# Optimization experiments

Measured on AMD Instinct MI355X. Metric: run time of the kernel, lower is better.

## Reference

```python
import jax, jax.numpy as jnp
import numpy as np
from jax import lax

B, H, W = 32, 40, 256
FREQ = 40            # freq_num
WIND = 0.5           # wind_size (seconds)
KF = 5               # input_filter_kernel (odd -> 'same' length)
CNN_OUT = 64 * 36 * 252  # out_channels[-1] * (H-4) * (W-4)


def setup_inputs() -> dict:
    key = jax.random.key(0)
    ks = jax.random.split(key, 9)
    return {
        "inputs": jax.random.normal(ks[0], (B, 1, H, W), jnp.float32),
        "w0": jax.random.normal(ks[1], (32, 1, 3, 3), jnp.float32) * 0.1,
        "b0": jax.random.normal(ks[2], (32,), jnp.float32) * 0.05,
        "w1": jax.random.normal(ks[3], (64, 32, 3, 3), jnp.float32) * 0.05,
        "b1": jax.random.normal(ks[4], (64,), jnp.float32) * 0.05,
        "wf": jax.random.normal(ks[5], (1, 1, 1, KF), jnp.float32) * 0.2,
        "bf": jax.random.normal(ks[6], (1,), jnp.float32) * 0.05,
        "wr": jax.random.normal(ks[7], (FREQ, CNN_OUT), jnp.float32) * 1e-3,
        "br": jax.random.normal(ks[8], (FREQ,), jnp.float32) * 0.05,
    }


def _conv2d(x, w, padding):
    return lax.conv_general_dilated(
        x, w, window_strides=(1, 1), padding=padding,
        dimension_numbers=("NCHW", "OIHW", "NCHW"))


def reference(inputs, w0, b0, w1, b1, wf, bf, wr, br):
    b, _, h, w_len = inputs.shape
    # input_filter: Conv1d(1,1,KF, padding=KF//2) applied independently per
    # frequency row -> equivalent to a 2D conv with a (1,KF) kernel.
    p = KF // 2
    feats = _conv2d(inputs, wf, [(0, 0), (p, p)]) + bf[None, :, None, None]  # [B,1,H,W]

    # conv stack with ReLU
    x = jax.nn.relu(_conv2d(inputs, w0, "VALID") + b0[None, :, None, None])
    x = jax.nn.relu(_conv2d(x, w1, "VALID") + b1[None, :, None, None])

    gates = jax.nn.sigmoid(x.reshape(b, -1) @ wr.T + br)

    fs = (1.0 / WIND) * jnp.linspace(1.0, FREQ, FREQ)          # [FREQ]
    wtd_mean_mod = jnp.mean(gates * fs[None, :])               # scalar

    # Fused modulation transform: instead of the per-frequency python loop
    # with materialized [B,H,W] broadcasts, compute sin/cos bases [FREQ,W]
    # and reduce over time with a single einsum each.
    t = jnp.linspace(0.0, WIND, w_len)                          # [W]
    phase = (2.0 * np.pi) * fs[:, None] * t[None, :]            # [FREQ,W]
    f0 = feats[:, 0]                                            # [B,H,W]
    inv_w = jnp.float32(1.0 / w_len)
    sins = jnp.einsum("fw,bhw->bfh", jnp.sin(phase), f0) * inv_w  # mean over W
    coss = jnp.einsum("fw,bhw->bfh", jnp.cos(phase), f0) * inv_w
    mag = jnp.sqrt(sins * sins + coss * coss)                   # [B,FREQ,H]
    mods = (mag * gates[:, :, None]).reshape(b, FREQ * h)       # cat over freq, dim=1
    return mods, wtd_mean_mod
```

## Files before the change

### kernel.cpp

```cpp
#include <hip/hip_runtime.h>
#include <hip/hip_bf16.h>
#include <math.h>

#define BB   32
#define HH   40
#define WW   256
#define NF   40
#define H1N  36
#define W1N  252
#define KCNN 580608
#define NW2  2016
#define KPW  288

typedef __attribute__((ext_vector_type(8))) short bf16x8;
typedef __attribute__((ext_vector_type(4))) float f32x4;

static __device__ __forceinline__ unsigned short f2bf(float v) {
    __hip_bfloat16 h = __float2bfloat16(v);
    return *(unsigned short*)&h;
}

static __device__ __forceinline__ bf16x8 packbf(float4 lo, float4 hi) {
    bf16x8 r;
    r[0] = (short)f2bf(lo.x); r[1] = (short)f2bf(lo.y);
    r[2] = (short)f2bf(lo.z); r[3] = (short)f2bf(lo.w);
    r[4] = (short)f2bf(hi.x); r[5] = (short)f2bf(hi.y);
    r[6] = (short)f2bf(hi.z); r[7] = (short)f2bf(hi.w);
    return r;
}

__global__ void k0_prep_w1(const float* __restrict__ w1, unsigned short* __restrict__ w1c) {
    int o = blockIdx.x * 256 + threadIdx.x;
    int c0  = o & 31;
    int c1  = (o >> 5) & 63;
    int tap = o >> 11;
    w1c[o] = f2bf(w1[(c1 * 32 + c0) * 9 + tap]);
}

__global__ __launch_bounds__(256) void k1_conv(
        const float* __restrict__ inp, const float* __restrict__ w0,
        const float* __restrict__ b0, const unsigned short* __restrict__ w1c,
        const float* __restrict__ b1, unsigned short* __restrict__ xbf) {
    __shared__ float ins[8 * 68];
    __shared__ __align__(16) unsigned short y0T[396 * 40];

    const int jt = blockIdx.x;
    const int it = blockIdx.y;
    const int b  = blockIdx.z;
    const int i0 = it * 4;
    const int j0 = jt * 64;
    const int tid = threadIdx.x;

    for (int s = tid; s < 544; s += 256) {
        int r = s / 68, c = s - r * 68;
        int gc = j0 + c;
        ins[s] = (gc < WW) ? inp[(b * HH + i0 + r) * WW + gc] : 0.0f;
    }
    __syncthreads();

    {
        const int c0 = tid & 31;
        const int pg = tid >> 5;
        float wreg[9];
        #pragma unroll
        for (int k = 0; k < 9; ++k) wreg[k] = w0[c0 * 9 + k];
        const float bias = b0[c0];
        for (int it2 = 0; it2 < 50; ++it2) {
            int pos = it2 * 8 + pg;
            if (pos < 396) {
                int r   = pos / 66;
                int col = pos - r * 66;
                float v = 0.0f;
                if (j0 + col < 254) {
                    float a = bias;
                    #pragma unroll
                    for (int ki = 0; ki < 3; ++ki)
                        #pragma unroll
                        for (int kj = 0; kj < 3; ++kj)
                            a = fmaf(ins[(r + ki) * 68 + col + kj], wreg[ki * 3 + kj], a);
                    v = fmaxf(a, 0.0f);
                }
                y0T[pos * 40 + c0] = f2bf(v);
            }
        }
    }
    __syncthreads();

    const int w    = tid >> 6;
    const int lane = tid & 63;
    const int l15  = lane & 15;
    const int quad = lane >> 4;

    float biasr[4][4];
    #pragma unroll
    for (int mt = 0; mt < 4; ++mt)
        #pragma unroll
        for (int rg = 0; rg < 4; ++rg)
            biasr[mt][rg] = b1[mt * 16 + quad * 4 + rg];

    f32x4 acc[4][4];
    #pragma unroll
    for (int mt = 0; mt < 4; ++mt)
        #pragma unroll
        for (int nt = 0; nt < 4; ++nt)
            acc[mt][nt] = (f32x4){0.f, 0.f, 0.f, 0.f};

    #pragma unroll
    for (int ki = 0; ki < 3; ++ki) {
        #pragma unroll
        for (int kj = 0; kj < 3; ++kj) {
            const int tap = ki * 3 + kj;
            bf16x8 af[4], bfr[4];
            #pragma unroll
            for (int mt = 0; mt < 4; ++mt)
                af[mt] = *(const bf16x8*)(w1c + ((tap * 64 + mt * 16 + l15) * 32 + quad * 8));
            #pragma unroll
            for (int nt = 0; nt < 4; ++nt)
                bfr[nt] = *(const bf16x8*)(y0T + (((w + ki) * 66 + nt * 16 + l15 + kj) * 40 + quad * 8));
            #pragma unroll
            for (int mt = 0; mt < 4; ++mt)
                #pragma unroll
                for (int nt = 0; nt < 4; ++nt)
                    acc[mt][nt] = __builtin_amdgcn_mfma_f32_16x16x32_bf16(
                        af[mt], bfr[nt], acc[mt][nt], 0, 0, 0);
        }
    }

    const int irow = i0 + w;
    #pragma unroll
    for (int nt = 0; nt < 4; ++nt) {
        const int j = j0 + nt * 16 + l15;
        if (j < W1N) {
            #pragma unroll
            for (int mt = 0; mt < 4; ++mt) {
                #pragma unroll
                for (int rg = 0; rg < 4; ++rg) {
                    int c1 = mt * 16 + quad * 4 + rg;
                    float v = fmaxf(acc[mt][nt][rg] + biasr[mt][rg], 0.0f);
                    xbf[(size_t)b * KCNN + (c1 * H1N + irow) * W1N + j] = f2bf(v);
                }
            }
        }
    }
}

__global__ __launch_bounds__(512) void k2_gemm(
        const unsigned short* __restrict__ xbf, const float* __restrict__ wr,
        float* __restrict__ gacc) {
    __shared__ float red[8][32][41];

    const int tid  = threadIdx.x;
    const int wv   = tid >> 6;
    const int lane = tid & 63;
    const int l15  = lane & 15;
    const int quad = lane >> 4;
    const size_t kw = (size_t)(blockIdx.x * 8 + wv) * KPW;

    const unsigned short* ap0 = xbf + (size_t)l15 * KCNN + kw + quad * 8;
    const unsigned short* ap1 = ap0 + (size_t)16 * KCNN;
    const float* bp0 = wr + (size_t)l15 * KCNN + kw + quad * 8;
    const float* bp1 = bp0 + (size_t)16 * KCNN;
    const bool v2 = (l15 < 8);
    const float* bp2 = bp0 + (size_t)32 * KCNN;

    f32x4 acc[2][3];
    #pragma unroll
    for (int mt = 0; mt < 2; ++mt)
        #pragma unroll
        for (int nt = 0; nt < 3; ++nt)
            acc[mt][nt] = (f32x4){0.f, 0.f, 0.f, 0.f};

    const float4 fz = {0.f, 0.f, 0.f, 0.f};
    bf16x8 a0c, a1c, a0n, a1n;
    float4 bw[3][2], bwn[3][2];

    a0c = *(const bf16x8*)ap0;
    a1c = *(const bf16x8*)ap1;
    bw[0][0] = *(const float4*)bp0; bw[0][1] = *(const float4*)(bp0 + 4);
    bw[1][0] = *(const float4*)bp1; bw[1][1] = *(const float4*)(bp1 + 4);
    if (v2) { bw[2][0] = *(const float4*)bp2; bw[2][1] = *(const float4*)(bp2 + 4); }
    else    { bw[2][0] = fz; bw[2][1] = fz; }

    for (int c = 0; c < 9; ++c) {
        if (c < 8) {
            const int o2 = (c + 1) * 32;
            a0n = *(const bf16x8*)(ap0 + o2);
            a1n = *(const bf16x8*)(ap1 + o2);
            bwn[0][0] = *(const float4*)(bp0 + o2); bwn[0][1] = *(const float4*)(bp0 + o2 + 4);
            bwn[1][0] = *(const float4*)(bp1 + o2); bwn[1][1] = *(const float4*)(bp1 + o2 + 4);
            if (v2) { bwn[2][0] = *(const float4*)(bp2 + o2); bwn[2][1] = *(const float4*)(bp2 + o2 + 4); }
            else    { bwn[2][0] = fz; bwn[2][1] = fz; }
        }
        #pragma unroll
        for (int nt = 0; nt < 3; ++nt) {
            bf16x8 bfrag = packbf(bw[nt][0], bw[nt][1]);
            acc[0][nt] = __builtin_amdgcn_mfma_f32_16x16x32_bf16(a0c, bfrag, acc[0][nt], 0, 0, 0);
            acc[1][nt] = __builtin_amdgcn_mfma_f32_16x16x32_bf16(a1c, bfrag, acc[1][nt], 0, 0, 0);
        }
        if (c < 8) {
            a0c = a0n; a1c = a1n;
            #pragma unroll
            for (int nt = 0; nt < 3; ++nt) { bw[nt][0] = bwn[nt][0]; bw[nt][1] = bwn[nt][1]; }
        }
    }

    #pragma unroll
    for (int mt = 0; mt < 2; ++mt)
        #pragma unroll
        for (int nt = 0; nt < 3; ++nt)
            #pragma unroll
            for (int rg = 0; rg < 4; ++rg) {
                int bb = mt * 16 + quad * 4 + rg;
                int ff = nt * 16 + l15;
                if (ff < NF) red[wv][bb][ff] = acc[mt][nt][rg];
            }
    __syncthreads();
    for (int p = tid; p < 1280; p += 512) {
        int bb = p / 40, ff = p - bb * 40;
        float s = 0.0f;
        #pragma unroll
        for (int w = 0; w < 8; ++w) s += red[w][bb][ff];
        atomicAdd(gacc + p, s);
    }
}

__global__ void k3_gates(const float* __restrict__ gacc, const float* __restrict__ br,
                         float* __restrict__ gates, float* __restrict__ out) {
    int p = blockIdx.x * 64 + threadIdx.x;
    int f = p % 40;
    float g = 1.0f / (1.0f + __expf(-(gacc[p] + br[f])));
    gates[p] = g;
    float fs = 2.0f * (float)(f + 1);
    atomicAdd(out + 51200, g * fs * (1.0f / 1280.0f));
}

__global__ __launch_bounds__(320) void k4_mods(
        const float* __restrict__ inp, const float* __restrict__ wf,
        const float* __restrict__ bfp, const float* __restrict__ gates,
        float* __restrict__ out) {
    const int f = blockIdx.x, b = blockIdx.y;
    const int tid = threadIdx.x;
    const int h  = tid >> 3;
    const int wl = tid & 7;
    float wfv[5];
    #pragma unroll
    for (int t = 0; t < 5; ++t) wfv[t] = wf[t];
    const float bias = bfp[0];
    const float cph = 6.283185307179586f * (float)(f + 1) / 255.0f;
    const float* row = inp + (b * HH + h) * WW;
    float sa = 0.0f, ca = 0.0f;
    for (int m = 0; m < 32; ++m) {
        int w = wl + 8 * m;
        float feat = bias;
        #pragma unroll
        for (int d = -2; d <= 2; ++d) {
            int wc = w + d;
            if (wc >= 0 && wc < WW) feat = fmaf(row[wc], wfv[d + 2], feat);
        }
        float sv, cv;
        __sincosf(cph * (float)w, &sv, &cv);
        sa = fmaf(sv, feat, sa);
        ca = fmaf(cv, feat, ca);
    }
    #pragma unroll
    for (int off = 4; off >= 1; off >>= 1) {
        sa += __shfl_xor(sa, off, 8);
        ca += __shfl_xor(ca, off, 8);
    }
    if (wl == 0) {
        float mag = sqrtf(sa * sa + ca * ca) * (1.0f / 256.0f);
        out[b * 1600 + f * 40 + h] = mag * gates[b * 40 + f];
    }
}

extern "C" void kernel_launch(void* const* d_in, const int* in_sizes, int n_in,
                              void* d_out, int out_size, void* d_ws, size_t ws_size,
                              hipStream_t stream) {
    const float* inp = (const float*)d_in[0];
    const float* w0  = (const float*)d_in[1];
    const float* b0  = (const float*)d_in[2];
    const float* w1  = (const float*)d_in[3];
    const float* b1  = (const float*)d_in[4];
    const float* wf  = (const float*)d_in[5];
    const float* bf_ = (const float*)d_in[6];
    const float* wr  = (const float*)d_in[7];
    const float* br  = (const float*)d_in[8];
    float* out = (float*)d_out;

    char* ws = (char*)d_ws;
    unsigned short* xbf = (unsigned short*)ws;
    unsigned short* w1c = (unsigned short*)(ws + 37158912);
    float* gacc  = (float*)(ws + 37195776);
    float* gates = (float*)(ws + 37200896);

    k0_prep_w1<<<72, 256, 0, stream>>>(w1, w1c);
    hipMemsetAsync(gacc, 0, 1280 * 4, stream);
    hipMemsetAsync(out + 51200, 0, 4, stream);
    k1_conv<<<dim3(4, 9, 32), 256, 0, stream>>>(inp, w0, b0, w1c, b1, xbf);
    k2_gemm<<<252, 512, 0, stream>>>(xbf, wr, gacc);
    k3_gates<<<20, 64, 0, stream>>>(gacc, br, gates, out);
    k4_mods<<<dim3(40, 32), 320, 0, stream>>>(inp, wf, bf_, gates, out);
}
```

Before: 233.0 us.

## Fuse gate epilogue into GEMM, stage conv output through LDS, drop memsets

Several changes land together. The gates/sigmoid kernel and both memsets are removed: k0 zeroes the accumulators, and the last-finishing GEMM block, found through an atomic counter, computes the gates and the weighted mean. The conv1 output is staged in shared memory and written with vectorized coalesced stores instead of scattered 2-byte stores. Conv0 now uses a register sliding window over rows, and the GEMM uses 504 blocks of 256 threads with branch-free loads on the third weight tile. These aim to cut launch overhead and uncoalesced global writes, at the cost of a serialized tail in one block and extra syncs.

```diff
diff --git a/kernel.cpp b/kernel.cpp
--- a/kernel.cpp
+++ b/kernel.cpp
@@ -9,7 +9,7 @@
 #define H1N  36
 #define W1N  252
 #define KCNN 580608
-#define NW2  2016
+#define NBLK2 504
 #define KPW  288
 
 typedef __attribute__((ext_vector_type(8))) short bf16x8;
@@ -29,20 +29,27 @@
     return r;
 }
 
-__global__ void k0_prep_w1(const float* __restrict__ w1, unsigned short* __restrict__ w1c) {
+__global__ void k0_prep(const float* __restrict__ w1, unsigned short* __restrict__ w1c,
+                        float* __restrict__ gacc, unsigned int* __restrict__ done) {
     int o = blockIdx.x * 256 + threadIdx.x;
     int c0  = o & 31;
     int c1  = (o >> 5) & 63;
     int tap = o >> 11;
     w1c[o] = f2bf(w1[(c1 * 32 + c0) * 9 + tap]);
+    if (blockIdx.x == 71) {
+        for (int p = threadIdx.x; p < 1280; p += 256) gacc[p] = 0.0f;
+        if (threadIdx.x == 0) *done = 0u;
+    }
 }
 
 __global__ __launch_bounds__(256) void k1_conv(
         const float* __restrict__ inp, const float* __restrict__ w0,
         const float* __restrict__ b0, const unsigned short* __restrict__ w1c,
         const float* __restrict__ b1, unsigned short* __restrict__ xbf) {
-    __shared__ float ins[8 * 68];
-    __shared__ __align__(16) unsigned short y0T[396 * 40];
+    __shared__ __align__(16) unsigned short smem[18432];
+    unsigned short* y0T = smem;
+    float* ins = (float*)(smem + 15840);
+    unsigned short* xp = smem;
 
     const int jt = blockIdx.x;
     const int it = blockIdx.y;
@@ -51,36 +58,60 @@
     const int j0 = jt * 64;
     const int tid = threadIdx.x;
 
-    for (int s = tid; s < 544; s += 256) {
+    for (int s = tid; s < 546; s += 256) {
         int r = s / 68, c = s - r * 68;
-        int gc = j0 + c;
-        ins[s] = (gc < WW) ? inp[(b * HH + i0 + r) * WW + gc] : 0.0f;
+        float v = 0.0f;
+        if (r < 8 && (j0 + c) < WW) v = inp[(b * HH + i0 + r) * WW + j0 + c];
+        ins[s] = v;
     }
     __syncthreads();
 
     {
-        const int c0 = tid & 31;
-        const int pg = tid >> 5;
+        const int c0  = tid & 31;
+        const int sub = tid >> 5;
         float wreg[9];
         #pragma unroll
         for (int k = 0; k < 9; ++k) wreg[k] = w0[c0 * 9 + k];
         const float bias = b0[c0];
-        for (int it2 = 0; it2 < 50; ++it2) {
-            int pos = it2 * 8 + pg;
-            if (pos < 396) {
-                int r   = pos / 66;
-                int col = pos - r * 66;
-                float v = 0.0f;
-                if (j0 + col < 254) {
-                    float a = bias;
+        for (int s = sub; s < 17; s += 8) {
+            const int cbase = 4 * s;
+            float rows[3][6];
+            #pragma unroll
+            for (int r = 0; r < 8; ++r) {
+                {
+                    const float4 a  = *(const float4*)&ins[r * 68 + cbase];
+                    const float2 b2 = *(const float2*)&ins[r * 68 + cbase + 4];
+                    float* dst = rows[r % 3];
+                    dst[0] = a.x; dst[1] = a.y; dst[2] = a.z;
+                    dst[3] = a.w; dst[4] = b2.x; dst[5] = b2.y;
+                }
+                if (r >= 2) {
+                    const int ro = r - 2;
+                    const float* r0 = rows[ro % 3];
+                    const float* r1 = rows[(ro + 1) % 3];
+                    const float* r2 = rows[(ro + 2) % 3];
                     #pragma unroll
-                    for (int ki = 0; ki < 3; ++ki)
-                        #pragma unroll
-                        for (int kj = 0; kj < 3; ++kj)
-                            a = fmaf(ins[(r + ki) * 68 + col + kj], wreg[ki * 3 + kj], a);
-                    v = fmaxf(a, 0.0f);
+                    for (int c = 0; c < 4; ++c) {
+                        const int colg = cbase + c;
+                        if (colg < 66) {
+                            float v = 0.0f;
+                            if (j0 + colg < 254) {
+                                float a = bias;
+                                a = fmaf(r0[c],     wreg[0], a);
+                                a = fmaf(r0[c + 1], wreg[1], a);
+                                a = fmaf(r0[c + 2], wreg[2], a);
+                                a = fmaf(r1[c],     wreg[3], a);
+                                a = fmaf(r1[c + 1], wreg[4], a);
+                                a = fmaf(r1[c + 2], wreg[5], a);
+                                a = fmaf(r2[c],     wreg[6], a);
+                                a = fmaf(r2[c + 1], wreg[7], a);
+                                a = fmaf(r2[c + 2], wreg[8], a);
+                                v = fmaxf(a, 0.0f);
+                            }
+                            y0T[(ro * 66 + colg) * 40 + c0] = f2bf(v);
+                        }
+                    }
                 }
-                y0T[pos * 40 + c0] = f2bf(v);
             }
         }
     }
@@ -125,43 +156,66 @@
                         af[mt], bfr[nt], acc[mt][nt], 0, 0, 0);
         }
     }
-
-    const int irow = i0 + w;
+    __syncthreads();
+
     #pragma unroll
     for (int nt = 0; nt < 4; ++nt) {
-        const int j = j0 + nt * 16 + l15;
-        if (j < W1N) {
-            #pragma unroll
-            for (int mt = 0; mt < 4; ++mt) {
-                #pragma unroll
-                for (int rg = 0; rg < 4; ++rg) {
-                    int c1 = mt * 16 + quad * 4 + rg;
-                    float v = fmaxf(acc[mt][nt][rg] + biasr[mt][rg], 0.0f);
-                    xbf[(size_t)b * KCNN + (c1 * H1N + irow) * W1N + j] = f2bf(v);
-                }
+        const int j = nt * 16 + l15;
+        #pragma unroll
+        for (int mt = 0; mt < 4; ++mt) {
+            #pragma unroll
+            for (int rg = 0; rg < 4; ++rg) {
+                const int c1 = mt * 16 + quad * 4 + rg;
+                const float v = fmaxf(acc[mt][nt][rg] + biasr[mt][rg], 0.0f);
+                xp[(c1 * 4 + w) * 72 + j] = f2bf(v);
             }
         }
     }
-}
-
-__global__ __launch_bounds__(512) void k2_gemm(
+    __syncthreads();
+    {
+        const int chunk = tid & 7;
+        const int rb    = tid >> 3;
+        #pragma unroll
+        for (int p = 0; p < 8; ++p) {
+            const int rowid = rb + 32 * p;
+            const int c1 = rowid >> 2, ci = rowid & 3;
+            uint4 v = *(const uint4*)&xp[rowid * 72 + chunk * 8];
+            const int gj = j0 + chunk * 8;
+            unsigned short* gp = xbf + (size_t)b * KCNN
+                               + (size_t)(c1 * H1N + i0 + ci) * W1N + gj;
+            uint2 lo; lo.x = v.x; lo.y = v.y;
+            if (gj + 8 <= W1N) {
+                uint2 hi; hi.x = v.z; hi.y = v.w;
+                *(uint2*)gp = lo;
+                *(uint2*)(gp + 4) = hi;
+            } else if (gj < W1N) {
+                *(uint2*)gp = lo;
+            }
+        }
+    }
+}
+
+__global__ __launch_bounds__(256) void k2_gemm(
         const unsigned short* __restrict__ xbf, const float* __restrict__ wr,
-        float* __restrict__ gacc) {
-    __shared__ float red[8][32][41];
+        const float* __restrict__ br, float* __restrict__ gacc,
+        unsigned int* __restrict__ done, float* __restrict__ gates,
+        float* __restrict__ out) {
+    __shared__ float red[4][32][41];
+    __shared__ unsigned int lastf;
 
     const int tid  = threadIdx.x;
     const int wv   = tid >> 6;
     const int lane = tid & 63;
     const int l15  = lane & 15;
     const int quad = lane >> 4;
-    const size_t kw = (size_t)(blockIdx.x * 8 + wv) * KPW;
+    const size_t kw = (size_t)(blockIdx.x * 4 + wv) * KPW;
 
     const unsigned short* ap0 = xbf + (size_t)l15 * KCNN + kw + quad * 8;
     const unsigned short* ap1 = ap0 + (size_t)16 * KCNN;
     const float* bp0 = wr + (size_t)l15 * KCNN + kw + quad * 8;
     const float* bp1 = bp0 + (size_t)16 * KCNN;
-    const bool v2 = (l15 < 8);
-    const float* bp2 = bp0 + (size_t)32 * KCNN;
+    const int r2 = (l15 < 8) ? (32 + l15) : 39;
+    const float* bp2 = wr + (size_t)r2 * KCNN + kw + quad * 8;
 
     f32x4 acc[2][3];
     #pragma unroll
@@ -170,7 +224,6 @@
         for (int nt = 0; nt < 3; ++nt)
             acc[mt][nt] = (f32x4){0.f, 0.f, 0.f, 0.f};
 
-    const float4 fz = {0.f, 0.f, 0.f, 0.f};
     bf16x8 a0c, a1c, a0n, a1n;
     float4 bw[3][2], bwn[3][2];
 
@@ -178,8 +231,7 @@
     a1c = *(const bf16x8*)ap1;
     bw[0][0] = *(const float4*)bp0; bw[0][1] = *(const float4*)(bp0 + 4);
     bw[1][0] = *(const float4*)bp1; bw[1][1] = *(const float4*)(bp1 + 4);
-    if (v2) { bw[2][0] = *(const float4*)bp2; bw[2][1] = *(const float4*)(bp2 + 4); }
-    else    { bw[2][0] = fz; bw[2][1] = fz; }
+    bw[2][0] = *(const float4*)bp2; bw[2][1] = *(const float4*)(bp2 + 4);
 
     for (int c = 0; c < 9; ++c) {
         if (c < 8) {
@@ -188,8 +240,7 @@
             a1n = *(const bf16x8*)(ap1 + o2);
             bwn[0][0] = *(const float4*)(bp0 + o2); bwn[0][1] = *(const float4*)(bp0 + o2 + 4);
             bwn[1][0] = *(const float4*)(bp1 + o2); bwn[1][1] = *(const float4*)(bp1 + o2 + 4);
-            if (v2) { bwn[2][0] = *(const float4*)(bp2 + o2); bwn[2][1] = *(const float4*)(bp2 + o2 + 4); }
-            else    { bwn[2][0] = fz; bwn[2][1] = fz; }
+            bwn[2][0] = *(const float4*)(bp2 + o2); bwn[2][1] = *(const float4*)(bp2 + o2 + 4);
         }
         #pragma unroll
         for (int nt = 0; nt < 3; ++nt) {
@@ -215,23 +266,35 @@
                 if (ff < NF) red[wv][bb][ff] = acc[mt][nt][rg];
             }
     __syncthreads();
-    for (int p = tid; p < 1280; p += 512) {
+    for (int p = tid; p < 1280; p += 256) {
         int bb = p / 40, ff = p - bb * 40;
-        float s = 0.0f;
-        #pragma unroll
-        for (int w = 0; w < 8; ++w) s += red[w][bb][ff];
-        atomicAdd(gacc + p, s);
-    }
-}
-
-__global__ void k3_gates(const float* __restrict__ gacc, const float* __restrict__ br,
-                         float* __restrict__ gates, float* __restrict__ out) {
-    int p = blockIdx.x * 64 + threadIdx.x;
-    int f = p % 40;
-    float g = 1.0f / (1.0f + __expf(-(gacc[p] + br[f])));
-    gates[p] = g;
-    float fs = 2.0f * (float)(f + 1);
-    atomicAdd(out + 51200, g * fs * (1.0f / 1280.0f));
+        atomicAdd(gacc + p, red[0][bb][ff] + red[1][bb][ff] + red[2][bb][ff] + red[3][bb][ff]);
+    }
+    __syncthreads();
+
+    if (tid == 0) {
+        __threadfence();
+        lastf = (atomicAdd(done, 1u) == NBLK2 - 1) ? 1u : 0u;
+    }
+    __syncthreads();
+    if (lastf) {
+        __threadfence();
+        float part = 0.0f;
+        for (int p = tid; p < 1280; p += 256) {
+            float s = __hip_atomic_load(gacc + p, __ATOMIC_RELAXED, __HIP_MEMORY_SCOPE_AGENT);
+            int f = p % 40;
+            float g = 1.0f / (1.0f + __expf(-(s + br[f])));
+            gates[p] = g;
+            part += g * 2.0f * (float)(f + 1);
+        }
+        #pragma unroll
+        for (int off = 32; off >= 1; off >>= 1) part += __shfl_xor(part, off);
+        float* redf = (float*)red;
+        if ((tid & 63) == 0) redf[tid >> 6] = part;
+        __syncthreads();
+        if (tid == 0)
+            out[51200] = (redf[0] + redf[1] + redf[2] + redf[3]) * (1.0f / 1280.0f);
+    }
 }
 
 __global__ __launch_bounds__(320) void k4_mods(
@@ -292,12 +355,10 @@
     unsigned short* w1c = (unsigned short*)(ws + 37158912);
     float* gacc  = (float*)(ws + 37195776);
     float* gates = (float*)(ws + 37200896);
-
-    k0_prep_w1<<<72, 256, 0, stream>>>(w1, w1c);
-    hipMemsetAsync(gacc, 0, 1280 * 4, stream);
-    hipMemsetAsync(out + 51200, 0, 4, stream);
+    unsigned int* done = (unsigned int*)(ws + 37206016);
+
+    k0_prep<<<72, 256, 0, stream>>>(w1, w1c, gacc, done);
     k1_conv<<<dim3(4, 9, 32), 256, 0, stream>>>(inp, w0, b0, w1c, b1, xbf);
-    k2_gemm<<<252, 512, 0, stream>>>(xbf, wr, gacc);
-    k3_gates<<<20, 64, 0, stream>>>(gacc, br, gates, out);
+    k2_gemm<<<NBLK2, 256, 0, stream>>>(xbf, wr, br, gacc, done, gates, out);
     k4_mods<<<dim3(40, 32), 320, 0, stream>>>(inp, wf, bf_, gates, out);
 }
```

After: 238.1 us. 2.2% more time.
